# Optimization experiments

Hardware: AMD Instinct MI355X
Metric: run time of the kernel (lower is better)

The kernel has to match this reference:

```python
import jax, jax.numpy as jnp
import numpy as np

NA, H, DIN, E, NN, ED = 1024, 128, 172, 256, 100000, 1
REG = 0.1
_gl_nodes = np.array([-0.1834346424956498, -0.525532409916329, -0.7966664774136267, -0.9602898564975363,
                      0.1834346424956498, 0.525532409916329, 0.7966664774136267, 0.9602898564975363], np.float32)
_gl_w = np.array([0.362683783378362, 0.3137066458778873, 0.2223810344533745, 0.1012285362903763] * 2, np.float32)
T_NODES = jnp.asarray(0.5 * (_gl_nodes + 1.0))    # tau = 1.0
T_WEIGHTS = jnp.asarray(0.5 * _gl_w)


def _rmsnorm(x, scale, eps=1e-8):
    rms = jnp.sqrt(jnp.sum(x * x, axis=-1, keepdims=True)) / np.sqrt(x.shape[-1])
    return scale * x / (rms + eps)


def setup_inputs() -> dict:
    key = jax.random.key(0)
    ks = jax.random.split(key, 16)
    s = 0.02
    return {
        "L_agg": 0.1 * jax.random.normal(ks[0], (NA, NA), jnp.float32),
        "delta_L_agg": 0.1 * jax.random.normal(ks[1], (NA, NA), jnp.float32),
        "x_sub": jax.random.normal(ks[2], (NA, DIN), jnp.float32),
        "m1_vec": jax.random.normal(ks[3], (NN, H), jnp.float32),
        "m2_vec": jax.random.normal(ks[4], (NN, H), jnp.float32),
        "names_table": jnp.zeros((NN, ED), jnp.float32),  # typ='Nil' static embedding
        "rms1_scale": jnp.ones((H,), jnp.float32),
        "rms2_scale": jnp.ones((H,), jnp.float32),
        "W_tune": s * jax.random.normal(ks[5], (DIN + 2 * ED, H), jnp.float32),
        "b_tune": jnp.zeros((H,), jnp.float32),
        "W_B1": s * jax.random.normal(ks[6], (H, H), jnp.float32),
        "b_B1": jnp.zeros((H,), jnp.float32),
        "W_B2": s * jax.random.normal(ks[7], (H, H), jnp.float32),
        "b_B2": jnp.zeros((H,), jnp.float32),
        "W_dt": 0.01 * jax.random.normal(ks[8], (H, 1), jnp.float32),
        "b_dt": -3.0 + 0.5 * jax.random.normal(ks[9], (1,), jnp.float32),  # softplus(b) small, like _init_dt_bias
        "A_log_1": jax.random.normal(ks[10], (H,), jnp.float32),
        "A_log_2": jax.random.normal(ks[11], (H,), jnp.float32),
        "target_src": jax.random.randint(ks[12], (E,), 0, NN),
        "target_dst": jax.random.randint(ks[13], (E,), 0, NN),
        "active_input_ids": jax.random.randint(ks[14], (NA,), 0, NN),
    }


def reference(L_agg, delta_L_agg, x_sub, m1_vec, m2_vec, names_table,
              rms1_scale, rms2_scale, W_tune, b_tune, W_B1, b_B1, W_B2, b_B2,
              W_dt, b_dt, A_log_1, A_log_2, target_src, target_dst, active_input_ids):
    n = L_agg.shape[0]
    I = jnp.eye(n, dtype=L_agg.dtype)
    # ZOH discretization of the graph Laplacian operator
    As_bar = I - REG * delta_L_agg + REG ** 2 * (delta_L_agg @ (L_agg + delta_L_agg / 2))
    dt = delta_L_agg[None] * T_NODES[:, None, None]                       # [8,n,n]
    LHS = I[None] - REG * dt + REG ** 2 * (dt @ (L_agg[None] + dt / 2))   # [8,n,n]
    P_L_inv = I - REG * L_agg
    # static-embedding neighbor info (zeros for 'Nil', done faithfully)
    neigh = jnp.zeros((n, 2 * ED), L_agg.dtype)
    neigh = neigh.at[:E, :ED].set(names_table[target_src])
    neigh = neigh.at[:E, ED:].set(names_table[target_dst])
    neigh = neigh.at[E:2 * E, :ED].set(names_table[target_dst])
    neigh = neigh.at[E:2 * E, ED:].set(names_table[target_src])
    x_in = jnp.concatenate([x_sub, neigh], axis=1)
    zt = x_in @ W_tune + b_tune                                           # TuneInput
    ztn = _rmsnorm(zt, rms1_scale)
    Bzt = ztn @ W_B1 + b_B1
    delta_1 = jax.nn.softplus(ztn @ W_dt + b_dt)                          # [n,1] broadcasts over H
    dA1 = delta_1 * (-jnp.exp(A_log_1))                                   # [n,H]
    At_bar_1 = jnp.exp(dA1)
    C_1 = (P_L_inv @ (Bzt * delta_1))[None] * T_WEIGHTS[:, None, None]    # [8,n,H]
    RHS_1 = jnp.exp(dA1[None] * T_NODES[:, None, None])                   # [8,n,H]
    integral_1 = jnp.sum((LHS @ C_1) * RHS_1, axis=0)                     # GL quadrature
    m1 = m1_vec[active_input_ids]
    updated_c_1 = As_bar @ (m1 * At_bar_1) + integral_1
    # second selective-SSM stage (reconstructed symmetrically from truncation)
    u_2 = zt + jax.nn.gelu(updated_c_1, approximate=True)
    u_2n = _rmsnorm(u_2, rms2_scale)
    But = u_2n @ W_B2 + b_B2
    delta_2 = jax.nn.softplus(u_2n @ W_dt + b_dt)
    dA2 = delta_2 * (-jnp.exp(A_log_2))
    At_bar_2 = jnp.exp(dA2)
    C_2 = (P_L_inv @ (But * delta_2))[None] * T_WEIGHTS[:, None, None]
    RHS_2 = jnp.exp(dA2[None] * T_NODES[:, None, None])
    integral_2 = jnp.sum((LHS @ C_2) * RHS_2, axis=0)
    m2 = m2_vec[active_input_ids]
    updated_c_2 = As_bar @ (m2 * At_bar_2) + integral_2
    return jnp.stack([updated_c_1, updated_c_2])                           # [2,n,H]
```

## Files before the change

### kernel.cpp

```cpp
#include <hip/hip_runtime.h>
#include <math.h>

#define N_A   1024
#define HDIM  128
#define DIN   172
#define E_CNT 256
#define LP    72

typedef __attribute__((ext_vector_type(8))) short bf16x8;
typedef __attribute__((ext_vector_type(4))) float f32x4;

__device__ __forceinline__ unsigned short f2bf(float x) {
    unsigned int u = __float_as_uint(x);
    unsigned int r = (u + 0x7fffu + ((u >> 16) & 1u)) >> 16;
    return (unsigned short)r;
}
__device__ __forceinline__ float bf2f(unsigned short x) {
    return __uint_as_float((unsigned int)x << 16);
}

__constant__ float c_t[8] = {
    0.4082826787521751f, 0.2372337950418355f, 0.10166676129318665f, 0.019855071751231843f,
    0.5917173212478249f, 0.7627662049581645f, 0.8983332387068134f, 0.9801449282487682f};
__constant__ float c_w[8] = {
    0.181341891689181f, 0.15685332293894365f, 0.11119051722668725f, 0.05061426814518815f,
    0.181341891689181f, 0.15685332293894365f, 0.11119051722668725f, 0.05061426814518815f};

__global__ __launch_bounds__(256)
void conv_all(const float* __restrict__ L, const float* __restrict__ dL,
              const float* __restrict__ x_sub, const float* __restrict__ names,
              const int* __restrict__ src, const int* __restrict__ dst,
              const float* __restrict__ W_tune, const float* __restrict__ b_tune,
              const float* __restrict__ W_B1, const float* __restrict__ W_B2,
              unsigned short* __restrict__ Lb, unsigned short* __restrict__ dLb,
              unsigned short* __restrict__ LbT, unsigned short* __restrict__ dLbT,
              unsigned short* __restrict__ WB1T, unsigned short* __restrict__ WB2T,
              float* __restrict__ zt)
{
    __shared__ unsigned short tl[64][72];
    const int b = blockIdx.x, tid = threadIdx.x;
    if (b < 2048) {
        const int t = b * 256 + tid;
        const float* s = (t < 262144) ? L : dL;
        unsigned short* d = (t < 262144) ? Lb : dLb;
        const int q = (t < 262144) ? t : t - 262144;
        float4 v = *(const float4*)(s + (size_t)q * 4);
        ushort4 o;
        o.x = f2bf(v.x); o.y = f2bf(v.y); o.z = f2bf(v.z); o.w = f2bf(v.w);
        *(ushort4*)(d + (size_t)q * 4) = o;
    } else if (b < 2176) {
        const int t = (b - 2048) * 256 + tid;
        const int half = t >> 14, tt = t & 16383;
        const int j = tt >> 7, k = tt & 127;
        (half ? WB2T : WB1T)[tt] = f2bf((half ? W_B2 : W_B1)[k * HDIM + j]);
    } else if (b < 2688) {
        const int t = b - 2176;
        const float* s = (t < 256) ? L : dL;
        unsigned short* d = (t < 256) ? LbT : dLbT;
        const int tile = t & 255, tr = tile >> 4, tc = tile & 15;
        const int row = tid >> 2, cg = (tid & 3) << 4;
        #pragma unroll
        for (int e = 0; e < 4; ++e) {
            float4 v = *(const float4*)(s + (size_t)(tr * 64 + row) * 1024 + tc * 64 + cg + e * 4);
            tl[row][cg + e * 4 + 0] = f2bf(v.x);
            tl[row][cg + e * 4 + 1] = f2bf(v.y);
            tl[row][cg + e * 4 + 2] = f2bf(v.z);
            tl[row][cg + e * 4 + 3] = f2bf(v.w);
        }
        __syncthreads();
        unsigned short* drow = d + (size_t)(tc * 64 + row) * 1024 + tr * 64 + cg;
        #pragma unroll
        for (int e = 0; e < 4; ++e) {
            ushort4 o;
            o.x = tl[cg + e * 4 + 0][row];
            o.y = tl[cg + e * 4 + 1][row];
            o.z = tl[cg + e * 4 + 2][row];
            o.w = tl[cg + e * 4 + 3][row];
            *(ushort4*)(drow + e * 4) = o;
        }
    } else {
        float* xl = (float*)tl;
        const int blk = b - 2688;
        const int g = tid >> 7, j = tid & 127;
        const int row = blk * 2 + g;
        for (int k = j; k < DIN + 2; k += 128) {
            float val;
            if (k < DIN) val = x_sub[(size_t)row * DIN + k];
            else if (k == DIN)
                val = (row < E_CNT) ? names[src[row]] :
                      (row < 2 * E_CNT) ? names[dst[row - E_CNT]] : 0.f;
            else
                val = (row < E_CNT) ? names[dst[row]] :
                      (row < 2 * E_CNT) ? names[src[row - E_CNT]] : 0.f;
            xl[g * 176 + k] = val;
        }
        __syncthreads();
        float acc = b_tune[j];
        #pragma unroll 2
        for (int k = 0; k < DIN + 2; ++k) acc += xl[g * 176 + k] * W_tune[k * HDIM + j];
        zt[(size_t)row * HDIM + j] = acc;
    }
}

__device__ __forceinline__ void core_sa(
    const unsigned short* __restrict__ ag, const unsigned short* __restrict__ bg,
    unsigned short* As, unsigned short* Bs, int klen,
    int srow, int skc, int wrow, int wcol, int fr, int fk, f32x4 (&acc)[2][2])
{
    bf16x8 pa0 = *(const bf16x8*)ag, pa1 = *(const bf16x8*)(ag + 8);
    bf16x8 pb0 = *(const bf16x8*)bg, pb1 = *(const bf16x8*)(bg + 8);
    for (int k0 = 0; k0 < klen; k0 += 64) {
        __syncthreads();
        *(bf16x8*)&As[srow * LP + skc] = pa0; *(bf16x8*)&As[srow * LP + skc + 8] = pa1;
        *(bf16x8*)&Bs[srow * LP + skc] = pb0; *(bf16x8*)&Bs[srow * LP + skc + 8] = pb1;
        __syncthreads();
        if (k0 + 64 < klen) {
            pa0 = *(const bf16x8*)(ag + k0 + 64); pa1 = *(const bf16x8*)(ag + k0 + 72);
            pb0 = *(const bf16x8*)(bg + k0 + 64); pb1 = *(const bf16x8*)(bg + k0 + 72);
        }
        #pragma unroll
        for (int h = 0; h < 2; ++h) {
            const int ko = h * 32 + fk;
            bf16x8 a0 = *(const bf16x8*)&As[(wrow + fr) * LP + ko];
            bf16x8 a1 = *(const bf16x8*)&As[(wrow + 16 + fr) * LP + ko];
            bf16x8 b0 = *(const bf16x8*)&Bs[(wcol + fr) * LP + ko];
            bf16x8 b1 = *(const bf16x8*)&Bs[(wcol + 16 + fr) * LP + ko];
            acc[0][0] = __builtin_amdgcn_mfma_f32_16x16x32_bf16(a0, b0, acc[0][0], 0, 0, 0);
            acc[0][1] = __builtin_amdgcn_mfma_f32_16x16x32_bf16(a0, b1, acc[0][1], 0, 0, 0);
            acc[1][0] = __builtin_amdgcn_mfma_f32_16x16x32_bf16(a1, b0, acc[1][0], 0, 0, 0);
            acc[1][1] = __builtin_amdgcn_mfma_f32_16x16x32_bf16(a1, b1, acc[1][1], 0, 0, 0);
        }
    }
}

__device__ __forceinline__ float rowsum128(float v, float* red, int j)
{
    #pragma unroll
    for (int o = 32; o > 0; o >>= 1) v += __shfl_xor(v, o, 64);
    if ((j & 63) == 0) red[j >> 6] = v;
    __syncthreads();
    const float t = red[0] + red[1];
    __syncthreads();
    return t;
}

__device__ __forceinline__ float post_elem(float y1, float y2, float y3, float s,
                                           float g, float u, float dA)
{
    const float bl = -0.1f * y1 + 0.01f * y2;
    const float cq = 0.005f * y3;
    float integ = 0.f;
    #pragma unroll
    for (int k = 0; k < 8; ++k) {
        const float t = c_t[k];
        integ += c_w[k] * (g + t * bl + t * t * cq) * expf(dA * t);
    }
    return u - 0.1f * s + integ;
}

__device__ void rmsbz_task(int rb, int tid,
    unsigned short* xnL , float* dltL , float* red ,
    const float* zt,
    const float* Gf, const float* dLVf, const float* P1Vf, const float* P2Vf,
    const float* dLUf, const float* P1Uf, const float* P2Uf,
    const float* dlt_prev, const float* A_prev, float* out0,
    const float* rms_scale, const float* W_dt, const float* b_dt,
    const float* A_log, const float* m_vec, const int* act,
    const unsigned short* WBT, const float* b_B,
    float* VU, unsigned short* VUt, float* Udst, int ustride,
    float* dlt_out)
{
    const int g = tid >> 7, j = tid & 127;

    #pragma unroll
    for (int rr = 0; rr < 2; ++rr) {
        const int lr = g * 2 + rr;
        const int row = rb * 4 + lr;
        const int idx = row * HDIM + j;
        float x;
        if (!out0) {
            x = zt[idx];
        } else {
            const float y1 = dLVf[idx] - 0.1f * P1Vf[idx];
            const float s  = dLUf[idx] - 0.1f * P1Uf[idx] - 0.05f * P2Uf[idx];
            const float dA = -dlt_prev[row] * expf(A_prev[j]);
            const float o1 = post_elem(y1, P1Vf[idx], P2Vf[idx], s, Gf[idx],
                                       VU[(size_t)row * 256 + 128 + j], dA);
            out0[idx] = o1;
            const float g3 = o1 * o1 * o1;
            const float gel = 0.5f * o1 * (1.0f + tanhf(0.7978845608028654f * (o1 + 0.044715f * g3)));
            x = zt[idx] + gel;
        }
        const float ss = rowsum128(x * x, red + 2 * g, j);
        const float rms = sqrtf(ss) * 0.08838834764831845f;
        const float xn = rms_scale[j] * x / (rms + 1e-8f);
        const float ds = rowsum128(xn * W_dt[j], red + 2 * g, j);
        const float dd = ds + b_dt[0];
        const float delta = dd > 0.f ? dd + log1pf(expf(-dd)) : log1pf(expf(dd));
        xnL[lr * 136 + j] = f2bf(xn);
        if (j == 0) { dltL[lr] = delta; dlt_out[row] = delta; }
        const float U = m_vec[(size_t)act[row] * HDIM + j] * expf(-delta * expf(A_log[j]));
        Udst[(size_t)row * ustride + j] = U;
        VUt[(size_t)(128 + j) * 1024 + row] = f2bf(U);
    }
    __syncthreads();

    const int lane = tid & 63, w = tid >> 6;
    const int fr = lane & 15, fg = lane >> 4, fk = fg << 3;
    #pragma unroll
    for (int n = 0; n < 2; ++n) {
        const int col = w * 32 + n * 16 + fr;
        f32x4 acc = {};
        #pragma unroll
        for (int ks = 0; ks < 4; ++ks) {
            const int ko = ks * 32 + fk;
            bf16x8 a = *(const bf16x8*)&xnL[fr * 136 + ko];
            bf16x8 b = *(const bf16x8*)(WBT + (size_t)col * HDIM + ko);
            acc = __builtin_amdgcn_mfma_f32_16x16x32_bf16(a, b, acc, 0, 0, 0);
        }
        if (fg == 0) {
            const float bb = b_B[col];
            float vv[4];
            #pragma unroll
            for (int r = 0; r < 4; ++r) {
                vv[r] = (acc[r] + bb) * dltL[r];
                VU[(size_t)(rb * 4 + r) * 256 + col] = vv[r];
            }
            ushort4 tv;
            tv.x = f2bf(vv[0]); tv.y = f2bf(vv[1]); tv.z = f2bf(vv[2]); tv.w = f2bf(vv[3]);
            *(ushort4*)&VUt[(size_t)col * 1024 + rb * 4] = tv;
        }
    }
}

__global__ __launch_bounds__(256)
void k_d2(const unsigned short* __restrict__ LbT, const unsigned short* __restrict__ dLbT,
          const unsigned short* __restrict__ dLb,
          unsigned short* __restrict__ P1b, unsigned short* __restrict__ P2b,
          const float* __restrict__ zt,
          const float* __restrict__ rms1, const float* __restrict__ W_dt,
          const float* __restrict__ b_dt, const float* __restrict__ A1,
          const float* __restrict__ m1, const int* __restrict__ act,
          const unsigned short* __restrict__ WB1T, const float* __restrict__ b_B1,
          float* __restrict__ VU, unsigned short* __restrict__ VUt,
          float* __restrict__ dlt1)
{
    __shared__ unsigned short shm[128 * LP];
    const int bid = blockIdx.x, tid = threadIdx.x;

    if (bid < 512) {
        unsigned short* As = shm; unsigned short* Bs = shm + 64 * LP;
        const int srow = tid >> 2, skc = (tid & 3) << 4;
        const int lane = tid & 63, w = tid >> 6;
        const int wrow = (w >> 1) * 32, wcol = (w & 1) * 32;
        const int fr = lane & 15, fg = lane >> 4, fk = fg << 3;
        const int bx = bid >> 4, rb = bid & 15;
        const int unit = bx >> 4, cb = bx & 15;
        const unsigned short* A = unit ? dLbT : LbT;
        unsigned short* O = unit ? P2b : P1b;
        const unsigned short* ag = A   + (size_t)(rb * 64 + srow) * 1024 + skc;
        const unsigned short* bg = dLb + (size_t)(cb * 64 + srow) * 1024 + skc;
        f32x4 acc[2][2] = {};
        core_sa(ag, bg, As, Bs, 1024, srow, skc, wrow, wcol, fr, fk, acc);
        #pragma unroll
        for (int m = 0; m < 2; ++m) {
            const int gm = rb * 64 + wrow + m * 16 + fg * 4;
            #pragma unroll
            for (int n = 0; n < 2; ++n) {
                const int gj = cb * 64 + wcol + n * 16 + fr;
                ushort4 tv;
                tv.x = f2bf(acc[m][n][0]); tv.y = f2bf(acc[m][n][1]);
                tv.z = f2bf(acc[m][n][2]); tv.w = f2bf(acc[m][n][3]);
                *(ushort4*)&O[(size_t)gj * 1024 + gm] = tv;
            }
        }
    } else {
        unsigned short* xnL = shm;
        float* dltL = (float*)(shm + 16 * 136);
        float* red  = dltL + 4;
        const int rb = bid - 512;
        rmsbz_task(rb, tid, xnL, dltL, red, zt,
                   nullptr, nullptr, nullptr, nullptr, nullptr, nullptr, nullptr,
                   nullptr, nullptr, nullptr,
                   rms1, W_dt, b_dt, A1, m1, act, WB1T, b_B1,
                   VU, VUt, VU + 128, 256, dlt1);
    }
}

__global__ __launch_bounds__(256)
void k_big(const unsigned short* __restrict__ Lb, const unsigned short* __restrict__ dLb,
           const unsigned short* __restrict__ P1b, const unsigned short* __restrict__ P2b,
           const unsigned short* __restrict__ VUt, const float* __restrict__ VU,
           float* __restrict__ Gf, float* __restrict__ dLVf, float* __restrict__ P1Vf,
           float* __restrict__ P2Vf, float* __restrict__ dLUf,
           float* __restrict__ P1Uf, float* __restrict__ P2Uf)
{
    __shared__ unsigned short shm[96 * LP];
    unsigned short* AsL = shm;
    unsigned short* Bs  = shm + 32 * LP;

    const int bid = blockIdx.x, tid = threadIdx.x;
    const int unit = bid >> 6, rem = bid & 63;
    const int rb = rem >> 1, cb = rem & 1;

    const unsigned short* A;
    float* O;
    switch (unit) {
        case 0: A = Lb;  O = Gf;   break;
        case 1: A = dLb; O = dLVf; break;
        case 2: A = P1b; O = P1Vf; break;
        case 3: A = P2b; O = P2Vf; break;
        case 4: A = dLb; O = dLUf; break;
        case 5: A = P1b; O = P1Uf; break;
        default: A = P2b; O = P2Uf; break;
    }
    const int bn0 = ((unit >= 4) ? 128 : 0) + cb * 64;

    const int sar = tid >> 3, sac = (tid & 7) << 3;
    const int sbr = tid >> 2, sbc = (tid & 3) << 4;

    const unsigned short* ag = A   + (size_t)(rb * 32 + sar) * 1024 + sac;
    const unsigned short* bg = VUt + (size_t)(bn0 + sbr) * 1024 + sbc;

    const int lane = tid & 63, w = tid >> 6;
    const int fr = lane & 15, fg = lane >> 4, fk = fg << 3;

    f32x4 acc[2] = {};
    bf16x8 pa = *(const bf16x8*)ag;
    bf16x8 pb0 = *(const bf16x8*)bg, pb1 = *(const bf16x8*)(bg + 8);

    for (int k0 = 0; k0 < 1024; k0 += 64) {
        __syncthreads();
        *(bf16x8*)&AsL[sar * LP + sac] = pa;
        *(bf16x8*)&Bs[sbr * LP + sbc] = pb0; *(bf16x8*)&Bs[sbr * LP + sbc + 8] = pb1;
        __syncthreads();
        if (k0 + 64 < 1024) {
            pa = *(const bf16x8*)(ag + k0 + 64);
            pb0 = *(const bf16x8*)(bg + k0 + 64); pb1 = *(const bf16x8*)(bg + k0 + 72);
        }
        #pragma unroll
        for (int h = 0; h < 2; ++h) {
            const int ko = h * 32 + fk;
            bf16x8 a0 = *(const bf16x8*)&AsL[fr * LP + ko];
            bf16x8 a1 = *(const bf16x8*)&AsL[(16 + fr) * LP + ko];
            bf16x8 b0 = *(const bf16x8*)&Bs[(w * 16 + fr) * LP + ko];
            acc[0] = __builtin_amdgcn_mfma_f32_16x16x32_bf16(a0, b0, acc[0], 0, 0, 0);
            acc[1] = __builtin_amdgcn_mfma_f32_16x16x32_bf16(a1, b0, acc[1], 0, 0, 0);
        }
    }

    #pragma unroll
    for (int m = 0; m < 2; ++m) {
        const int gm = rb * 32 + m * 16 + fg * 4;
        const int gj = cb * 64 + w * 16 + fr;
        if (unit == 0) {
            #pragma unroll
            for (int r = 0; r < 4; ++r)
                O[(size_t)(gm + r) * 128 + gj] =
                    VU[(size_t)(gm + r) * 256 + gj] - 0.1f * acc[m][r];
        } else {
            #pragma unroll
            for (int r = 0; r < 4; ++r)
                O[(size_t)(gm + r) * 128 + gj] = acc[m][r];
        }
    }
}

__global__ __launch_bounds__(256)
void k_mid(const float* __restrict__ Gf, const float* __restrict__ dLVf,
           const float* __restrict__ P1Vf, const float* __restrict__ P2Vf,
           const float* __restrict__ dLUf, const float* __restrict__ P1Uf,
           const float* __restrict__ P2Uf,
           const float* __restrict__ zt, const float* __restrict__ dlt1,
           const float* __restrict__ A1,
           const float* __restrict__ rms2, const float* __restrict__ W_dt,
           const float* __restrict__ b_dt, const float* __restrict__ A2,
           const float* __restrict__ m2, const int* __restrict__ act,
           const unsigned short* __restrict__ WB2T, const float* __restrict__ b_B2,
           float* __restrict__ VU, unsigned short* __restrict__ VUt,
           float* __restrict__ U2, float* __restrict__ dlt2,
           float* __restrict__ out0)
{
    __shared__ unsigned short shm[16 * 136 + 32];
    unsigned short* xnL = shm;
    float* dltL = (float*)(shm + 16 * 136);
    float* red  = dltL + 4;
    rmsbz_task(blockIdx.x, threadIdx.x, xnL, dltL, red, zt,
               Gf, dLVf, P1Vf, P2Vf, dLUf, P1Uf, P2Uf,
               dlt1, A1, out0,
               rms2, W_dt, b_dt, A2, m2, act, WB2T, b_B2,
               VU, VUt, U2, 128, dlt2);
}

__global__ __launch_bounds__(256)
void k_tail(const float* __restrict__ Gf, const float* __restrict__ dLVf,
            const float* __restrict__ P1Vf, const float* __restrict__ P2Vf,
            const float* __restrict__ dLUf, const float* __restrict__ P1Uf,
            const float* __restrict__ P2Uf,
            const float* __restrict__ U2, const float* __restrict__ dlt,
            const float* __restrict__ A_log, float* __restrict__ out)
{
    const int idx = blockIdx.x * 256 + threadIdx.x;
    const int i = idx >> 7, j = idx & 127;
    const float y1 = dLVf[idx] - 0.1f * P1Vf[idx];
    const float s  = dLUf[idx] - 0.1f * P1Uf[idx] - 0.05f * P2Uf[idx];
    const float dA = -dlt[i] * expf(A_log[j]);
    out[idx] = post_elem(y1, P1Vf[idx], P2Vf[idx], s, Gf[idx], U2[idx], dA);
}

extern "C" void kernel_launch(void* const* d_in, const int* in_sizes, int n_in,
                              void* d_out, int out_size, void* d_ws, size_t ws_size,
                              hipStream_t stream)
{
    const float* L      = (const float*)d_in[0];
    const float* dL     = (const float*)d_in[1];
    const float* x_sub  = (const float*)d_in[2];
    const float* m1     = (const float*)d_in[3];
    const float* m2     = (const float*)d_in[4];
    const float* names  = (const float*)d_in[5];
    const float* rms1   = (const float*)d_in[6];
    const float* rms2   = (const float*)d_in[7];
    const float* W_tune = (const float*)d_in[8];
    const float* b_tune = (const float*)d_in[9];
    const float* W_B1   = (const float*)d_in[10];
    const float* b_B1   = (const float*)d_in[11];
    const float* W_B2   = (const float*)d_in[12];
    const float* b_B2   = (const float*)d_in[13];
    const float* W_dt   = (const float*)d_in[14];
    const float* b_dt   = (const float*)d_in[15];
    const float* A1     = (const float*)d_in[16];
    const float* A2     = (const float*)d_in[17];
    const int*   src    = (const int*)d_in[18];
    const int*   dst    = (const int*)d_in[19];
    const int*   act    = (const int*)d_in[20];
    float* out = (float*)d_out;

    float* ws    = (float*)d_ws;
    float* zt    = ws;
    float* VU    = zt    + 131072;
    float* U2    = VU    + 262144;
    float* Gf    = U2    + 131072;
    float* dLVf  = Gf    + 131072;
    float* P1Vf  = dLVf  + 131072;
    float* P2Vf  = P1Vf  + 131072;
    float* dLUf  = P2Vf  + 131072;
    float* P1Uf  = dLUf  + 131072;
    float* P2Uf  = P1Uf  + 131072;
    float* dlt1  = P2Uf  + 131072;
    float* dlt2  = dlt1  + 1024;
    unsigned short* Lb    = (unsigned short*)(dlt2 + 1024);
    unsigned short* dLb   = Lb    + 1048576;
    unsigned short* LbT   = dLb   + 1048576;
    unsigned short* dLbT  = LbT   + 1048576;
    unsigned short* P1b   = dLbT  + 1048576;
    unsigned short* P2b   = P1b   + 1048576;
    unsigned short* VUt   = P2b   + 1048576;
    unsigned short* WB1T  = VUt   + 262144;
    unsigned short* WB2T  = WB1T  + 16384;

    conv_all<<<dim3(3200), dim3(256), 0, stream>>>(
        L, dL, x_sub, names, src, dst, W_tune, b_tune, W_B1, W_B2,
        Lb, dLb, LbT, dLbT, WB1T, WB2T, zt);

    k_d2<<<dim3(768), dim3(256), 0, stream>>>(
        LbT, dLbT, dLb, P1b, P2b, zt,
        rms1, W_dt, b_dt, A1, m1, act, WB1T, b_B1,
        VU, VUt, dlt1);

    k_big<<<dim3(448), dim3(256), 0, stream>>>(
        Lb, dLb, P1b, P2b, VUt, VU,
        Gf, dLVf, P1Vf, P2Vf, dLUf, P1Uf, P2Uf);

    k_mid<<<dim3(256), dim3(256), 0, stream>>>(
        Gf, dLVf, P1Vf, P2Vf, dLUf, P1Uf, P2Uf,
        zt, dlt1, A1, rms2, W_dt, b_dt, A2, m2, act,
        WB2T, b_B2, VU, VUt, U2, dlt2, out);

    k_big<<<dim3(448), dim3(256), 0, stream>>>(
        Lb, dLb, P1b, P2b, VUt, VU,
        Gf, dLVf, P1Vf, P2Vf, dLUf, P1Uf, P2Uf);

    k_tail<<<dim3(512), dim3(256), 0, stream>>>(
        Gf, dLVf, P1Vf, P2Vf, dLUf, P1Uf, P2Uf,
        U2, dlt2, A2, out + 131072);
}
```

Before: 82.21 us.

## Move input projection to bf16 MFMA GEMM and split stage-1 prep kernel

```diff
diff --git a/kernel.cpp b/kernel.cpp
--- a/kernel.cpp
+++ b/kernel.cpp
@@ -30,12 +30,12 @@
 void conv_all(const float* __restrict__ L, const float* __restrict__ dL,
               const float* __restrict__ x_sub, const float* __restrict__ names,
               const int* __restrict__ src, const int* __restrict__ dst,
-              const float* __restrict__ W_tune, const float* __restrict__ b_tune,
-              const float* __restrict__ W_B1, const float* __restrict__ W_B2,
+              const float* __restrict__ W_tune, const float* __restrict__ W_B1,
+              const float* __restrict__ W_B2,
               unsigned short* __restrict__ Lb, unsigned short* __restrict__ dLb,
               unsigned short* __restrict__ LbT, unsigned short* __restrict__ dLbT,
-              unsigned short* __restrict__ WB1T, unsigned short* __restrict__ WB2T,
-              float* __restrict__ zt)
+              unsigned short* __restrict__ Xb, unsigned short* __restrict__ WtT,
+              unsigned short* __restrict__ WB1T, unsigned short* __restrict__ WB2T)
 {
     __shared__ unsigned short tl[64][72];
     const int b = blockIdx.x, tid = threadIdx.x;
@@ -48,13 +48,30 @@
         ushort4 o;
         o.x = f2bf(v.x); o.y = f2bf(v.y); o.z = f2bf(v.z); o.w = f2bf(v.w);
         *(ushort4*)(d + (size_t)q * 4) = o;
-    } else if (b < 2176) {
+    } else if (b < 2816) {
         const int t = (b - 2048) * 256 + tid;
+        const int i = t / 192, k = t - i * 192;
+        float val = 0.f;
+        if (k < DIN) val = x_sub[(size_t)i * DIN + k];
+        else if (k == DIN) {
+            if (i < E_CNT)          val = names[src[i]];
+            else if (i < 2 * E_CNT) val = names[dst[i - E_CNT]];
+        } else if (k == DIN + 1) {
+            if (i < E_CNT)          val = names[dst[i]];
+            else if (i < 2 * E_CNT) val = names[src[i - E_CNT]];
+        }
+        Xb[t] = f2bf(val);
+    } else if (b < 2912) {
+        const int t = (b - 2816) * 256 + tid;
+        const int j = t / 192, k = t - j * 192;
+        WtT[t] = (k < DIN + 2) ? f2bf(W_tune[k * HDIM + j]) : (unsigned short)0;
+    } else if (b < 3040) {
+        const int t = (b - 2912) * 256 + tid;
         const int half = t >> 14, tt = t & 16383;
         const int j = tt >> 7, k = tt & 127;
         (half ? WB2T : WB1T)[tt] = f2bf((half ? W_B2 : W_B1)[k * HDIM + j]);
-    } else if (b < 2688) {
-        const int t = b - 2176;
+    } else {
+        const int t = b - 3040;
         const float* s = (t < 256) ? L : dL;
         unsigned short* d = (t < 256) ? LbT : dLbT;
         const int tile = t & 255, tr = tile >> 4, tc = tile & 15;
@@ -78,27 +95,6 @@
             o.w = tl[cg + e * 4 + 3][row];
             *(ushort4*)(drow + e * 4) = o;
         }
-    } else {
-        float* xl = (float*)tl;
-        const int blk = b - 2688;
-        const int g = tid >> 7, j = tid & 127;
-        const int row = blk * 2 + g;
-        for (int k = j; k < DIN + 2; k += 128) {
-            float val;
-            if (k < DIN) val = x_sub[(size_t)row * DIN + k];
-            else if (k == DIN)
-                val = (row < E_CNT) ? names[src[row]] :
-                      (row < 2 * E_CNT) ? names[dst[row - E_CNT]] : 0.f;
-            else
-                val = (row < E_CNT) ? names[dst[row]] :
-                      (row < 2 * E_CNT) ? names[src[row - E_CNT]] : 0.f;
-            xl[g * 176 + k] = val;
-        }
-        __syncthreads();
-        float acc = b_tune[j];
-        #pragma unroll 2
-        for (int k = 0; k < DIN + 2; ++k) acc += xl[g * 176 + k] * W_tune[k * HDIM + j];
-        zt[(size_t)row * HDIM + j] = acc;
     }
 }
 
@@ -129,6 +125,64 @@
             acc[0][1] = __builtin_amdgcn_mfma_f32_16x16x32_bf16(a0, b1, acc[0][1], 0, 0, 0);
             acc[1][0] = __builtin_amdgcn_mfma_f32_16x16x32_bf16(a1, b0, acc[1][0], 0, 0, 0);
             acc[1][1] = __builtin_amdgcn_mfma_f32_16x16x32_bf16(a1, b1, acc[1][1], 0, 0, 0);
+        }
+    }
+}
+
+__global__ __launch_bounds__(256)
+void k_d2(const unsigned short* __restrict__ LbT, const unsigned short* __restrict__ dLbT,
+          const unsigned short* __restrict__ dLb,
+          unsigned short* __restrict__ P1b, unsigned short* __restrict__ P2b,
+          const unsigned short* __restrict__ Xb, const unsigned short* __restrict__ WtT,
+          const float* __restrict__ b_tune, float* __restrict__ zt)
+{
+    __shared__ unsigned short shm[128 * LP];
+    unsigned short* As = shm; unsigned short* Bs = shm + 64 * LP;
+    const int bid = blockIdx.x, tid = threadIdx.x;
+    const int srow = tid >> 2, skc = (tid & 3) << 4;
+    const int lane = tid & 63, w = tid >> 6;
+    const int wrow = (w >> 1) * 32, wcol = (w & 1) * 32;
+    const int fr = lane & 15, fg = lane >> 4, fk = fg << 3;
+
+    if (bid < 512) {
+        const int bx = bid >> 4, rb = bid & 15;
+        const int unit = bx >> 4, cb = bx & 15;
+        const unsigned short* A = unit ? dLbT : LbT;
+        unsigned short* O = unit ? P2b : P1b;
+        const unsigned short* ag = A   + (size_t)(rb * 64 + srow) * 1024 + skc;
+        const unsigned short* bg = dLb + (size_t)(cb * 64 + srow) * 1024 + skc;
+        f32x4 acc[2][2] = {};
+        core_sa(ag, bg, As, Bs, 1024, srow, skc, wrow, wcol, fr, fk, acc);
+        #pragma unroll
+        for (int m = 0; m < 2; ++m) {
+            const int gm = rb * 64 + wrow + m * 16 + fg * 4;
+            #pragma unroll
+            for (int n = 0; n < 2; ++n) {
+                const int gj = cb * 64 + wcol + n * 16 + fr;
+                ushort4 tv;
+                tv.x = f2bf(acc[m][n][0]); tv.y = f2bf(acc[m][n][1]);
+                tv.z = f2bf(acc[m][n][2]); tv.w = f2bf(acc[m][n][3]);
+                *(ushort4*)&O[(size_t)gj * 1024 + gm] = tv;
+            }
+        }
+    } else {
+        const int t = bid - 512;
+        const int cb = t >> 4, rb = t & 15;
+        const unsigned short* ag = Xb  + (size_t)(rb * 64 + srow) * 192 + skc;
+        const unsigned short* bg = WtT + (size_t)(cb * 64 + srow) * 192 + skc;
+        f32x4 acc[2][2] = {};
+        core_sa(ag, bg, As, Bs, 192, srow, skc, wrow, wcol, fr, fk, acc);
+        #pragma unroll
+        for (int m = 0; m < 2; ++m) {
+            const int gm = rb * 64 + wrow + m * 16 + fg * 4;
+            #pragma unroll
+            for (int n = 0; n < 2; ++n) {
+                const int gj = cb * 64 + wcol + n * 16 + fr;
+                const float bb = b_tune[gj];
+                #pragma unroll
+                for (int r = 0; r < 4; ++r)
+                    zt[(size_t)(gm + r) * HDIM + gj] = acc[m][n][r] + bb;
+            }
         }
     }
 }
@@ -234,57 +288,23 @@
 }
 
 __global__ __launch_bounds__(256)
-void k_d2(const unsigned short* __restrict__ LbT, const unsigned short* __restrict__ dLbT,
-          const unsigned short* __restrict__ dLb,
-          unsigned short* __restrict__ P1b, unsigned short* __restrict__ P2b,
-          const float* __restrict__ zt,
-          const float* __restrict__ rms1, const float* __restrict__ W_dt,
-          const float* __restrict__ b_dt, const float* __restrict__ A1,
-          const float* __restrict__ m1, const int* __restrict__ act,
-          const unsigned short* __restrict__ WB1T, const float* __restrict__ b_B1,
-          float* __restrict__ VU, unsigned short* __restrict__ VUt,
-          float* __restrict__ dlt1)
-{
-    __shared__ unsigned short shm[128 * LP];
-    const int bid = blockIdx.x, tid = threadIdx.x;
-
-    if (bid < 512) {
-        unsigned short* As = shm; unsigned short* Bs = shm + 64 * LP;
-        const int srow = tid >> 2, skc = (tid & 3) << 4;
-        const int lane = tid & 63, w = tid >> 6;
-        const int wrow = (w >> 1) * 32, wcol = (w & 1) * 32;
-        const int fr = lane & 15, fg = lane >> 4, fk = fg << 3;
-        const int bx = bid >> 4, rb = bid & 15;
-        const int unit = bx >> 4, cb = bx & 15;
-        const unsigned short* A = unit ? dLbT : LbT;
-        unsigned short* O = unit ? P2b : P1b;
-        const unsigned short* ag = A   + (size_t)(rb * 64 + srow) * 1024 + skc;
-        const unsigned short* bg = dLb + (size_t)(cb * 64 + srow) * 1024 + skc;
-        f32x4 acc[2][2] = {};
-        core_sa(ag, bg, As, Bs, 1024, srow, skc, wrow, wcol, fr, fk, acc);
-        #pragma unroll
-        for (int m = 0; m < 2; ++m) {
-            const int gm = rb * 64 + wrow + m * 16 + fg * 4;
-            #pragma unroll
-            for (int n = 0; n < 2; ++n) {
-                const int gj = cb * 64 + wcol + n * 16 + fr;
-                ushort4 tv;
-                tv.x = f2bf(acc[m][n][0]); tv.y = f2bf(acc[m][n][1]);
-                tv.z = f2bf(acc[m][n][2]); tv.w = f2bf(acc[m][n][3]);
-                *(ushort4*)&O[(size_t)gj * 1024 + gm] = tv;
-            }
-        }
-    } else {
-        unsigned short* xnL = shm;
-        float* dltL = (float*)(shm + 16 * 136);
-        float* red  = dltL + 4;
-        const int rb = bid - 512;
-        rmsbz_task(rb, tid, xnL, dltL, red, zt,
-                   nullptr, nullptr, nullptr, nullptr, nullptr, nullptr, nullptr,
-                   nullptr, nullptr, nullptr,
-                   rms1, W_dt, b_dt, A1, m1, act, WB1T, b_B1,
-                   VU, VUt, VU + 128, 256, dlt1);
-    }
+void k_rb1(const float* __restrict__ zt,
+           const float* __restrict__ rms1, const float* __restrict__ W_dt,
+           const float* __restrict__ b_dt, const float* __restrict__ A1,
+           const float* __restrict__ m1, const int* __restrict__ act,
+           const unsigned short* __restrict__ WB1T, const float* __restrict__ b_B1,
+           float* __restrict__ VU, unsigned short* __restrict__ VUt,
+           float* __restrict__ dlt1)
+{
+    __shared__ unsigned short shm[16 * 136 + 32];
+    unsigned short* xnL = shm;
+    float* dltL = (float*)(shm + 16 * 136);
+    float* red  = dltL + 4;
+    rmsbz_task(blockIdx.x, threadIdx.x, xnL, dltL, red, zt,
+               nullptr, nullptr, nullptr, nullptr, nullptr, nullptr, nullptr,
+               nullptr, nullptr, nullptr,
+               rms1, W_dt, b_dt, A1, m1, act, WB1T, b_B1,
+               VU, VUt, VU + 128, 256, dlt1);
 }
 
 __global__ __launch_bounds__(256)
@@ -455,17 +475,20 @@
     unsigned short* P1b   = dLbT  + 1048576;
     unsigned short* P2b   = P1b   + 1048576;
     unsigned short* VUt   = P2b   + 1048576;
-    unsigned short* WB1T  = VUt   + 262144;
+    unsigned short* Xb    = VUt   + 262144;
+    unsigned short* WtT   = Xb    + 196608;
+    unsigned short* WB1T  = WtT   + 24576;
     unsigned short* WB2T  = WB1T  + 16384;
 
-    conv_all<<<dim3(3200), dim3(256), 0, stream>>>(
-        L, dL, x_sub, names, src, dst, W_tune, b_tune, W_B1, W_B2,
-        Lb, dLb, LbT, dLbT, WB1T, WB2T, zt);
-
-    k_d2<<<dim3(768), dim3(256), 0, stream>>>(
-        LbT, dLbT, dLb, P1b, P2b, zt,
-        rms1, W_dt, b_dt, A1, m1, act, WB1T, b_B1,
-        VU, VUt, dlt1);
+    conv_all<<<dim3(3552), dim3(256), 0, stream>>>(
+        L, dL, x_sub, names, src, dst, W_tune, W_B1, W_B2,
+        Lb, dLb, LbT, dLbT, Xb, WtT, WB1T, WB2T);
+
+    k_d2<<<dim3(544), dim3(256), 0, stream>>>(
+        LbT, dLbT, dLb, P1b, P2b, Xb, WtT, b_tune, zt);
+
+    k_rb1<<<dim3(256), dim3(256), 0, stream>>>(
+        zt, rms1, W_dt, b_dt, A1, m1, act, WB1T, b_B1, VU, VUt, dlt1);
 
     k_big<<<dim3(448), dim3(256), 0, stream>>>(
         Lb, dLb, P1b, P2b, VUt, VU,
```

New measurement: 67.01 us. 1.23x faster.
